# Performance work log

Measured on AMD Instinct MI355X. Metric: run time of the kernel, lower is better.

The kernel has to match this reference:

```python
import jax, jax.numpy as jnp
import numpy as np

BLOCK = 15  # block_size from __init__
EPS = 1e-6


def setup_inputs() -> dict:
    key = jax.random.key(0)
    kq, kk, kv = jax.random.split(key, 3)
    B, H, L, D = 4, 16, 4800, 64  # L divisible by BLOCK
    return {
        "q": jax.random.normal(kq, (B, H, L, D), dtype=jnp.float32),
        "k": jax.random.normal(kk, (B, H, L, D), dtype=jnp.float32),
        "v": jax.random.normal(kv, (B, H, L, D), dtype=jnp.float32),
    }


def reference(q, k, v):
    # RobustAttention: relu(q/k/v), then independent cosFormer-style causal
    # linear attention inside each length-block of size BLOCK.
    B, H, L, D = q.shape
    w = BLOCK
    nb = L // w  # L chosen divisible; original zeros any remainder
    q = jax.nn.relu(q).reshape(B, H, nb, w, D)
    k = jax.nn.relu(k).reshape(B, H, nb, w, D)
    v = jax.nn.relu(v).reshape(B, H, nb, w, D)

    # cos_reweight index: pi/2 * (1..w) / m with m = w (block length)
    idx = (jnp.pi / 2) * jnp.arange(1, w + 1, dtype=jnp.float32) / w  # [w]
    sin = jnp.sin(idx)[:, None]  # [w,1]
    cos = jnp.cos(idx)[:, None]
    q_ = jnp.concatenate([q * sin, q * cos], axis=-1)  # [B,H,nb,w,2D]
    k_ = jnp.concatenate([k * sin, k * cos], axis=-1)

    # cumsum of outer products == causal (lower-triangular) linear attention:
    # qkv[l] = sum_{j<=l} (q_[l].k_[j]) v[j]; denom[l] = sum_{j<=l} q_[l].k_[j]
    scores = jnp.einsum('bhnqd,bhnkd->bhnqk', q_, k_)  # [B,H,nb,w,w]
    causal = jnp.tril(jnp.ones((w, w), dtype=bool))
    scores = jnp.where(causal, scores, jnp.float32(0))
    denom = jnp.maximum(scores.sum(-1), EPS)  # clamp_min(.., eps), [B,H,nb,w]
    out = jnp.einsum('bhnqk,bhnkd->bhnqd', scores, v) / denom[..., None]
    return out.reshape(B, H, L, D)
```

## Files before the change

kernel.cpp:

```cpp
#include <hip/hip_runtime.h>


namespace {

constexpr int W        = 15;
constexpr int CH       = 16;
constexpr int TILE4    = W * CH;
constexpr int TPW      = 4;
constexpr int NTHREADS = 64;
constexpr int RSTRIDE4 = CH + 1;
constexpr int TSTRIDE4 = W * RSTRIDE4;

typedef float f32x4_n __attribute__((ext_vector_type(4)));

__device__ __forceinline__ float4 relu4(float4 a) {
    return make_float4(fmaxf(a.x, 0.f), fmaxf(a.y, 0.f),
                       fmaxf(a.z, 0.f), fmaxf(a.w, 0.f));
}

__global__ __launch_bounds__(NTHREADS, 2)
void robust_attn_kernel(const float4* __restrict__ q4,
                        const float4* __restrict__ k4,
                        const float4* __restrict__ v4,
                        float4* __restrict__ o4,
                        int nblocks)
{
    __shared__ float4 slab[TPW * TSTRIDE4];

    const int tid  = threadIdx.x;
    const int lane = tid & 15;
    const int t    = tid >> 4;
    const int g0   = blockIdx.x * TPW;
    const int g    = g0 + t;
    const bool active = (g < nblocks);
    const bool ph1    = active && (lane < W);

    {
        const size_t base = (size_t)g0 * TILE4;
#pragma unroll
        for (int r = 0; r < (TPW * TILE4) / NTHREADS; ++r) {
            const int idx = tid + r * NTHREADS;
            const int tt  = idx / TILE4;
            const int pos = idx - tt * TILE4;
            const int rr  = pos >> 4;
            const int cc  = pos & 15;
            float4 x = make_float4(0.f, 0.f, 0.f, 0.f);
            if (g0 + tt < nblocks) x = q4[base + idx];
            slab[tt * TSTRIDE4 + rr * RSTRIDE4 + cc] = relu4(x);
        }
    }
    __syncthreads();

    float4 qr[CH];
    if (ph1) {
        const float4* __restrict__ ql = &slab[t * TSTRIDE4 + lane * RSTRIDE4];
#pragma unroll
        for (int c = 0; c < CH; ++c) qr[c] = ql[c];
    }
    __syncthreads();

    {
        const size_t base = (size_t)g0 * TILE4;
#pragma unroll
        for (int r = 0; r < (TPW * TILE4) / NTHREADS; ++r) {
            const int idx = tid + r * NTHREADS;
            const int tt  = idx / TILE4;
            const int pos = idx - tt * TILE4;
            const int rr  = pos >> 4;
            const int cc  = pos & 15;
            float4 x = make_float4(0.f, 0.f, 0.f, 0.f);
            if (g0 + tt < nblocks) x = k4[base + idx];
            slab[tt * TSTRIDE4 + rr * RSTRIDE4 + cc] = relu4(x);
        }
    }
    __syncthreads();

    float s[W];
#pragma unroll
    for (int j = 0; j < W; ++j) s[j] = 0.f;

    if (ph1) {
        const int l = lane;
        const float4* __restrict__ kl = &slab[t * TSTRIDE4];
#pragma unroll
        for (int j = 0; j < W; ++j) {
            float acc = 0.f;
#pragma unroll
            for (int c = 0; c < CH; ++c) {
                const float4 kk = kl[j * RSTRIDE4 + c];
                acc = fmaf(qr[c].x, kk.x, acc);
                acc = fmaf(qr[c].y, kk.y, acc);
                acc = fmaf(qr[c].z, kk.z, acc);
                acc = fmaf(qr[c].w, kk.w, acc);
            }
            s[j] = acc;
        }

        const float step = 1.57079632679489662f / (float)W;
        float denom = 0.f;
#pragma unroll
        for (int j = 0; j < W; ++j) {
            float wc = __cosf(step * (float)(l - j));
            float tv = (j <= l) ? s[j] * wc : 0.f;
            s[j] = tv;
            denom += tv;
        }
        const float inv = 1.f / fmaxf(denom, 1e-6f);
#pragma unroll
        for (int j = 0; j < W; ++j) s[j] *= inv;
    }

    if (active) {
        const float4* __restrict__ vp = v4 + (size_t)g * TILE4 + lane;
        float4* __restrict__ op       = o4 + (size_t)g * TILE4 + lane;

        float4 vv[W];
#pragma unroll
        for (int j = 0; j < W; ++j) vv[j] = relu4(vp[j * CH]);

        const int tbase = tid & 48;
#pragma unroll
        for (int l = 0; l < W; ++l) {
            float ax = 0.f, ay = 0.f, az = 0.f, aw = 0.f;
#pragma unroll
            for (int j = 0; j <= l; ++j) {
                const float w = __shfl(s[j], tbase + l, 64);
                ax = fmaf(w, vv[j].x, ax);
                ay = fmaf(w, vv[j].y, ay);
                az = fmaf(w, vv[j].z, az);
                aw = fmaf(w, vv[j].w, aw);
            }
            f32x4_n val = {ax, ay, az, aw};
            __builtin_nontemporal_store(val, (f32x4_n*)(op + l * CH));
        }
    }
}

}

extern "C" void kernel_launch(void* const* d_in, const int* in_sizes, int n_in,
                              void* d_out, int out_size, void* d_ws, size_t ws_size,
                              hipStream_t stream) {
    const float4* q = (const float4*)d_in[0];
    const float4* k = (const float4*)d_in[1];
    const float4* v = (const float4*)d_in[2];
    float4* out = (float4*)d_out;

    const int total   = in_sizes[0];
    const int nblocks = total / (W * CH * 4);
    const int wgs     = (nblocks + TPW - 1) / TPW;

    robust_attn_kernel<<<wgs, NTHREADS, 0, stream>>>(q, k, v, out, nblocks);
}
```

Before: 76.84 us.

## Double-buffer K tiles via async global-to-LDS loads across batches per workgroup

Each workgroup now loops over four batches of blocks. The next batch's K tile is prefetched into a second LDS buffer with global_load_lds while the current batch is computed. Q and V are read straight into registers instead of being staged through LDS, and ReLU is applied in place in LDS, which removes the block barriers. The aim is to hide load latency, but the grid shrinks to a quarter of its previous size with one wave per workgroup. That sharply cuts the number of waves in flight for a memory-bound kernel. Q reads also become strided per lane, and the code relies on implicit waits for the async LDS loads.

```diff
diff --git a/kernel.cpp b/kernel.cpp
--- a/kernel.cpp
+++ b/kernel.cpp
@@ -8,8 +8,10 @@
 constexpr int TILE4    = W * CH;
 constexpr int TPW      = 4;
 constexpr int NTHREADS = 64;
-constexpr int RSTRIDE4 = CH + 1;
-constexpr int TSTRIDE4 = W * RSTRIDE4;
+constexpr int ITERS    = 4;
+constexpr int SLOT4    = 258;
+constexpr int BUF4     = TPW * SLOT4;
+constexpr int BATCH4   = TPW * TILE4;
 
 typedef float f32x4_n __attribute__((ext_vector_type(4)));
 
@@ -18,121 +20,140 @@
                        fmaxf(a.z, 0.f), fmaxf(a.w, 0.f));
 }
 
-__global__ __launch_bounds__(NTHREADS, 2)
+__device__ __forceinline__ void gll16(const float4* g, float4* l) {
+    __builtin_amdgcn_global_load_lds(
+        (const __attribute__((address_space(1))) void*)g,
+        (__attribute__((address_space(3))) void*)l, 16, 0, 0);
+}
+
+__global__ __launch_bounds__(NTHREADS, 1)
 void robust_attn_kernel(const float4* __restrict__ q4,
                         const float4* __restrict__ k4,
                         const float4* __restrict__ v4,
                         float4* __restrict__ o4,
                         int nblocks)
 {
-    __shared__ float4 slab[TPW * TSTRIDE4];
+    __shared__ float4 slab[2 * BUF4];
 
-    const int tid  = threadIdx.x;
-    const int lane = tid & 15;
-    const int t    = tid >> 4;
-    const int g0   = blockIdx.x * TPW;
-    const int g    = g0 + t;
-    const bool active = (g < nblocks);
-    const bool ph1    = active && (lane < W);
+    const int tid      = threadIdx.x;
+    const int lane     = tid & 15;
+    const int t        = tid >> 4;
+    const int nbatches = (nblocks + TPW - 1) / TPW;
+    const int b0       = (int)blockIdx.x * ITERS;
+    const int limit4   = nblocks * TILE4;
 
-    {
-        const size_t base = (size_t)g0 * TILE4;
+    auto stage = [&](int batch, float4* sN) {
+        if (batch >= nbatches) return;
+        const int gbase = batch * BATCH4;
 #pragma unroll
-        for (int r = 0; r < (TPW * TILE4) / NTHREADS; ++r) {
+        for (int tt = 0; tt < TPW; ++tt) {
+#pragma unroll
+            for (int c = 0; c < 4; ++c) {
+                const int pos  = c * 64 + tid;
+                const int gidx = gbase + tt * TILE4 + pos;
+                if (pos < TILE4 && gidx < limit4)
+                    gll16(k4 + gidx, sN + tt * SLOT4 + pos);
+            }
+        }
+    };
+
+    auto body = [&](int batch, float4* sC, float4* sN) {
+        if (batch >= nbatches) return;
+        const int  g      = batch * TPW + t;
+        const bool active = (g < nblocks);
+        const bool ph1    = active && (lane < W);
+
+        float4 qraw[CH];
+        const float4* __restrict__ qp = q4 + (size_t)g * TILE4 + lane * CH;
+#pragma unroll
+        for (int c = 0; c < CH; ++c)
+            qraw[c] = active ? qp[c] : make_float4(0.f, 0.f, 0.f, 0.f);
+
+        float4 vraw[W];
+        const float4* __restrict__ vp = v4 + (size_t)g * TILE4 + lane;
+#pragma unroll
+        for (int j = 0; j < W; ++j)
+            vraw[j] = active ? vp[j * CH] : make_float4(0.f, 0.f, 0.f, 0.f);
+
+#pragma unroll
+        for (int r = 0; r < BATCH4 / NTHREADS; ++r) {
             const int idx = tid + r * NTHREADS;
             const int tt  = idx / TILE4;
             const int pos = idx - tt * TILE4;
-            const int rr  = pos >> 4;
-            const int cc  = pos & 15;
-            float4 x = make_float4(0.f, 0.f, 0.f, 0.f);
-            if (g0 + tt < nblocks) x = q4[base + idx];
-            slab[tt * TSTRIDE4 + rr * RSTRIDE4 + cc] = relu4(x);
-        }
-    }
-    __syncthreads();
-
-    float4 qr[CH];
-    if (ph1) {
-        const float4* __restrict__ ql = &slab[t * TSTRIDE4 + lane * RSTRIDE4];
-#pragma unroll
-        for (int c = 0; c < CH; ++c) qr[c] = ql[c];
-    }
-    __syncthreads();
-
-    {
-        const size_t base = (size_t)g0 * TILE4;
-#pragma unroll
-        for (int r = 0; r < (TPW * TILE4) / NTHREADS; ++r) {
-            const int idx = tid + r * NTHREADS;
-            const int tt  = idx / TILE4;
-            const int pos = idx - tt * TILE4;
-            const int rr  = pos >> 4;
-            const int cc  = pos & 15;
-            float4 x = make_float4(0.f, 0.f, 0.f, 0.f);
-            if (g0 + tt < nblocks) x = k4[base + idx];
-            slab[tt * TSTRIDE4 + rr * RSTRIDE4 + cc] = relu4(x);
-        }
-    }
-    __syncthreads();
-
-    float s[W];
-#pragma unroll
-    for (int j = 0; j < W; ++j) s[j] = 0.f;
-
-    if (ph1) {
-        const int l = lane;
-        const float4* __restrict__ kl = &slab[t * TSTRIDE4];
-#pragma unroll
-        for (int j = 0; j < W; ++j) {
-            float acc = 0.f;
-#pragma unroll
-            for (int c = 0; c < CH; ++c) {
-                const float4 kk = kl[j * RSTRIDE4 + c];
-                acc = fmaf(qr[c].x, kk.x, acc);
-                acc = fmaf(qr[c].y, kk.y, acc);
-                acc = fmaf(qr[c].z, kk.z, acc);
-                acc = fmaf(qr[c].w, kk.w, acc);
-            }
-            s[j] = acc;
+            float4* p = sC + tt * SLOT4 + pos;
+            *p = relu4(*p);
         }
 
-        const float step = 1.57079632679489662f / (float)W;
-        float denom = 0.f;
+        stage(batch + 1, sN);
+
+        float s[W];
 #pragma unroll
-        for (int j = 0; j < W; ++j) {
-            float wc = __cosf(step * (float)(l - j));
-            float tv = (j <= l) ? s[j] * wc : 0.f;
-            s[j] = tv;
-            denom += tv;
+        for (int j = 0; j < W; ++j) s[j] = 0.f;
+
+        if (ph1) {
+            float4 qr[CH];
+#pragma unroll
+            for (int c = 0; c < CH; ++c) qr[c] = relu4(qraw[c]);
+
+            const float4* __restrict__ kl = sC + t * SLOT4;
+#pragma unroll
+            for (int j = 0; j < W; ++j) {
+                float acc = 0.f;
+#pragma unroll
+                for (int c = 0; c < CH; ++c) {
+                    const float4 kk = kl[j * CH + c];
+                    acc = fmaf(qr[c].x, kk.x, acc);
+                    acc = fmaf(qr[c].y, kk.y, acc);
+                    acc = fmaf(qr[c].z, kk.z, acc);
+                    acc = fmaf(qr[c].w, kk.w, acc);
+                }
+                s[j] = acc;
+            }
+
+            const int   l    = lane;
+            const float step = 1.57079632679489662f / (float)W;
+            float denom = 0.f;
+#pragma unroll
+            for (int j = 0; j < W; ++j) {
+                float wc = __cosf(step * (float)(l - j));
+                float tv = (j <= l) ? s[j] * wc : 0.f;
+                s[j] = tv;
+                denom += tv;
+            }
+            const float inv = 1.f / fmaxf(denom, 1e-6f);
+#pragma unroll
+            for (int j = 0; j < W; ++j) s[j] *= inv;
         }
-        const float inv = 1.f / fmaxf(denom, 1e-6f);
+
+        if (active) {
+            float4* __restrict__ op = o4 + (size_t)g * TILE4 + lane;
+            const int tbase = tid & 48;
 #pragma unroll
-        for (int j = 0; j < W; ++j) s[j] *= inv;
-    }
+            for (int l = 0; l < W; ++l) {
+                float ax = 0.f, ay = 0.f, az = 0.f, aw = 0.f;
+#pragma unroll
+                for (int j = 0; j <= l; ++j) {
+                    const float w = __shfl(s[j], tbase + l, 64);
+                    const float4 vj = relu4(vraw[j]);
+                    ax = fmaf(w, vj.x, ax);
+                    ay = fmaf(w, vj.y, ay);
+                    az = fmaf(w, vj.z, az);
+                    aw = fmaf(w, vj.w, aw);
+                }
+                f32x4_n val = {ax, ay, az, aw};
+                __builtin_nontemporal_store(val, (f32x4_n*)(op + l * CH));
+            }
+        }
+    };
 
-    if (active) {
-        const float4* __restrict__ vp = v4 + (size_t)g * TILE4 + lane;
-        float4* __restrict__ op       = o4 + (size_t)g * TILE4 + lane;
+    float4* slabA = &slab[0];
+    float4* slabB = &slab[BUF4];
 
-        float4 vv[W];
+    stage(b0, slabA);
 #pragma unroll
-        for (int j = 0; j < W; ++j) vv[j] = relu4(vp[j * CH]);
-
-        const int tbase = tid & 48;
-#pragma unroll
-        for (int l = 0; l < W; ++l) {
-            float ax = 0.f, ay = 0.f, az = 0.f, aw = 0.f;
-#pragma unroll
-            for (int j = 0; j <= l; ++j) {
-                const float w = __shfl(s[j], tbase + l, 64);
-                ax = fmaf(w, vv[j].x, ax);
-                ay = fmaf(w, vv[j].y, ay);
-                az = fmaf(w, vv[j].z, az);
-                aw = fmaf(w, vv[j].w, aw);
-            }
-            f32x4_n val = {ax, ay, az, aw};
-            __builtin_nontemporal_store(val, (f32x4_n*)(op + l * CH));
-        }
+    for (int i = 0; i < ITERS; i += 2) {
+        body(b0 + i,     slabA, slabB);
+        body(b0 + i + 1, slabB, slabA);
     }
 }
 
@@ -146,9 +167,10 @@
     const float4* v = (const float4*)d_in[2];
     float4* out = (float4*)d_out;
 
-    const int total   = in_sizes[0];
-    const int nblocks = total / (W * CH * 4);
-    const int wgs     = (nblocks + TPW - 1) / TPW;
+    const int total    = in_sizes[0];
+    const int nblocks  = total / (W * CH * 4);
+    const int nbatches = (nblocks + TPW - 1) / TPW;
+    const int wgs      = (nbatches + ITERS - 1) / ITERS;
 
     robust_attn_kernel<<<wgs, NTHREADS, 0, stream>>>(q, k, v, out, nblocks);
 }
```

New measurement: 159.3 us. +107.3%, slower.
